# Optimization experiments

Measured on AMD Instinct MI355X. Metric: run time of the kernel, lower is better.

## Reference

```python
import jax, jax.numpy as jnp
import numpy as np

HIDDEN = 1024
B, S = 4, 2048

def setup_inputs() -> dict:
    key = jax.random.key(0)
    k1, k2 = jax.random.split(key)
    hidden_states = jax.random.normal(k1, (B, S, HIDDEN), dtype=jnp.float32)
    # torch nn.Linear weight layout: [out_features, in_features]
    W_proj = jax.random.normal(k2, (3 * HIDDEN, HIDDEN), dtype=jnp.float32) * (1.0 / np.sqrt(HIDDEN))
    b_proj = jnp.zeros((3 * HIDDEN,), dtype=jnp.float32)
    return {"hidden_states": hidden_states, "W_proj": W_proj, "b_proj": b_proj}

def reference(hidden_states, W_proj, b_proj):
    h = hidden_states.shape[-1]
    # fused QKV projection: y = x @ W^T + b
    qkv = jnp.einsum('bsh,oh->bso', hidden_states, W_proj) + b_proj
    q, k, v = jnp.split(qkv, 3, axis=-1)  # each [B,S,H]
    scale = 1.0 / jnp.sqrt(jnp.asarray(h, dtype=q.dtype))
    scores = jnp.einsum('bqh,bkh->bqk', q, k) * scale  # [B,S,S]
    attn = jax.nn.softmax(scores, axis=-1)
    out = jnp.einsum('bqk,bkh->bqh', attn, v)
    return out
```

## Files before the change

kernel.cpp:

```cpp
#include <hip/hip_runtime.h>
#include <stdint.h>

#define HIDDEN 1024
#define BATCH  4
#define SEQ    2048
#define TOKENS (BATCH * SEQ)
#define QKVD   (3 * HIDDEN)

typedef unsigned short u16;
typedef __attribute__((ext_vector_type(8))) short   short8;
typedef __attribute__((ext_vector_type(4))) float   floatx4;

__device__ __forceinline__ u16 f32_bf16_rne(float f) {
    unsigned int u = __float_as_uint(f);
    u += 0x7FFFu + ((u >> 16) & 1u);
    return (u16)(u >> 16);
}

__global__ __launch_bounds__(256) void cvt_bf16_kernel(
        const float* __restrict__ src, u16* __restrict__ dst, int n4) {
    int i = blockIdx.x * 256 + threadIdx.x;
    if (i >= n4) return;
    float4 v = ((const float4*)src)[i];
    ushort4 o;
    o.x = f32_bf16_rne(v.x); o.y = f32_bf16_rne(v.y);
    o.z = f32_bf16_rne(v.z); o.w = f32_bf16_rne(v.w);
    ((ushort4*)dst)[i] = o;
}

template <int EPI>
__global__ __launch_bounds__(256) void gemm_bt(
        const u16* __restrict__ A, const u16* __restrict__ B,
        void* __restrict__ Cv, const float* __restrict__ bias,
        int K, int lda, int ldb, int ldc,
        size_t sA, size_t sB, size_t sC, float scale) {
    __shared__ u16 As[128 * 32];
    __shared__ u16 Bs[128 * 32];

    const int t    = threadIdx.x;
    const int lane = t & 63;
    const int wid  = t >> 6;
    const int bm   = blockIdx.y * 128;
    const int bn   = blockIdx.x * 128;

    const u16* Ab = A + (size_t)blockIdx.z * sA;
    const u16* Bb = B + (size_t)blockIdx.z * sB;

    const int srow = lane >> 2;
    const int scol = ((lane & 3) ^ ((lane >> 3) & 3)) * 8;

    const int wm = (wid >> 1) * 64;
    const int wn = (wid & 1) * 64;
    const int fr = lane & 15;
    const int fc = lane >> 4;
    const int foff = fr * 32 + ((fc ^ ((fr >> 1) & 3)) * 8);

    floatx4 acc[4][4];
#pragma unroll
    for (int i = 0; i < 4; i++)
#pragma unroll
        for (int j = 0; j < 4; j++) acc[i][j] = (floatx4){0.f, 0.f, 0.f, 0.f};

    for (int k0 = 0; k0 < K; k0 += 32) {
        __syncthreads();
#pragma unroll
        for (int j = 0; j < 2; j++) {
            const int chunk = wid * 2 + j;
            const int rt = chunk * 16 + srow;
            const u16* ga = Ab + (size_t)(bm + rt) * lda + (k0 + scol);
            __builtin_amdgcn_global_load_lds(
                (const __attribute__((address_space(1))) void*)ga,
                (__attribute__((address_space(3))) void*)(&As[chunk * 512]),
                16, 0, 0);
            const u16* gb = Bb + (size_t)(bn + rt) * ldb + (k0 + scol);
            __builtin_amdgcn_global_load_lds(
                (const __attribute__((address_space(1))) void*)gb,
                (__attribute__((address_space(3))) void*)(&Bs[chunk * 512]),
                16, 0, 0);
        }
        __syncthreads();

        short8 af[4], bf[4];
#pragma unroll
        for (int mi = 0; mi < 4; mi++)
            af[mi] = *(const short8*)&As[((wm >> 4) + mi) * 512 + foff];
#pragma unroll
        for (int ni = 0; ni < 4; ni++)
            bf[ni] = *(const short8*)&Bs[((wn >> 4) + ni) * 512 + foff];
#pragma unroll
        for (int mi = 0; mi < 4; mi++)
#pragma unroll
            for (int ni = 0; ni < 4; ni++)
                acc[mi][ni] = __builtin_amdgcn_mfma_f32_16x16x32_bf16(
                    af[mi], bf[ni], acc[mi][ni], 0, 0, 0);
    }

    const int crow0 = bm + wm + (lane >> 4) * 4;
    const int ccol0 = bn + wn + fr;
    const size_t coff = (size_t)blockIdx.z * sC;

    if (EPI == 0) {
        u16* C = (u16*)Cv;
        float bv[4];
#pragma unroll
        for (int ni = 0; ni < 4; ni++) bv[ni] = bias[ccol0 + ni * 16];
#pragma unroll
        for (int mi = 0; mi < 4; mi++)
#pragma unroll
            for (int ni = 0; ni < 4; ni++)
#pragma unroll
                for (int r = 0; r < 4; r++)
                    C[coff + (size_t)(crow0 + mi * 16 + r) * ldc + (ccol0 + ni * 16)] =
                        f32_bf16_rne(acc[mi][ni][r] + bv[ni]);
    } else {
        float* C = (float*)Cv;
#pragma unroll
        for (int mi = 0; mi < 4; mi++)
#pragma unroll
            for (int ni = 0; ni < 4; ni++)
#pragma unroll
                for (int r = 0; r < 4; r++) {
                    float v = acc[mi][ni][r];
                    if (EPI == 1) v *= scale;
                    C[coff + (size_t)(crow0 + mi * 16 + r) * ldc + (ccol0 + ni * 16)] = v;
                }
    }
}

__global__ __launch_bounds__(256) void softmax_kernel(
        const float* __restrict__ S, u16* __restrict__ P) {
    __shared__ float redm[4];
    __shared__ float reds[4];
    const size_t base = (size_t)blockIdx.x * SEQ;
    const int t = threadIdx.x, lane = t & 63, wid = t >> 6;
    const float4* src = (const float4*)(S + base);
    float4 a = src[t], b = src[t + 256];

    float m = fmaxf(fmaxf(fmaxf(a.x, a.y), fmaxf(a.z, a.w)),
                    fmaxf(fmaxf(b.x, b.y), fmaxf(b.z, b.w)));
#pragma unroll
    for (int off = 32; off; off >>= 1) m = fmaxf(m, __shfl_xor(m, off, 64));
    if (lane == 0) redm[wid] = m;
    __syncthreads();
    m = fmaxf(fmaxf(redm[0], redm[1]), fmaxf(redm[2], redm[3]));

    float e[8];
    e[0] = __expf(a.x - m); e[1] = __expf(a.y - m);
    e[2] = __expf(a.z - m); e[3] = __expf(a.w - m);
    e[4] = __expf(b.x - m); e[5] = __expf(b.y - m);
    e[6] = __expf(b.z - m); e[7] = __expf(b.w - m);
    float s = e[0] + e[1] + e[2] + e[3] + e[4] + e[5] + e[6] + e[7];
#pragma unroll
    for (int off = 32; off; off >>= 1) s += __shfl_xor(s, off, 64);
    if (lane == 0) reds[wid] = s;
    __syncthreads();
    s = reds[0] + reds[1] + reds[2] + reds[3];
    const float r = 1.f / s;

    ushort4* dst = (ushort4*)(P + base);
    ushort4 o0, o1;
    o0.x = f32_bf16_rne(e[0] * r); o0.y = f32_bf16_rne(e[1] * r);
    o0.z = f32_bf16_rne(e[2] * r); o0.w = f32_bf16_rne(e[3] * r);
    o1.x = f32_bf16_rne(e[4] * r); o1.y = f32_bf16_rne(e[5] * r);
    o1.z = f32_bf16_rne(e[6] * r); o1.w = f32_bf16_rne(e[7] * r);
    dst[t] = o0;
    dst[t + 256] = o1;
}

__global__ __launch_bounds__(256) void transposeV_kernel(
        const u16* __restrict__ qkv, u16* __restrict__ Vt) {
    __shared__ u16 tile[64][66];
    const int b = blockIdx.z;
    const int s0 = blockIdx.x * 64, h0 = blockIdx.y * 64;
    const int t = threadIdx.x;
    const int c = t & 63, r4 = t >> 6;
#pragma unroll
    for (int i = 0; i < 16; i++) {
        int sl = i * 4 + r4;
        tile[sl][c] = qkv[(size_t)(b * SEQ + s0 + sl) * QKVD + 2 * HIDDEN + h0 + c];
    }
    __syncthreads();
#pragma unroll
    for (int i = 0; i < 16; i++) {
        int hl = i * 4 + r4;
        Vt[(size_t)(b * HIDDEN + h0 + hl) * SEQ + s0 + c] = tile[c][hl];
    }
}

extern "C" void kernel_launch(void* const* d_in, const int* in_sizes, int n_in,
                              void* d_out, int out_size, void* d_ws, size_t ws_size,
                              hipStream_t stream) {
    const float* x    = (const float*)d_in[0];
    const float* W    = (const float*)d_in[1];
    const float* bias = (const float*)d_in[2];
    float* out = (float*)d_out;

    u16* Xb  = (u16*)d_ws;
    u16* Wb  = Xb + (size_t)TOKENS * HIDDEN;
    u16* qkv = Wb + (size_t)QKVD * HIDDEN;
    float* scores = (float*)(qkv + (size_t)TOKENS * QKVD);
    u16* P  = (u16*)(scores + (size_t)BATCH * SEQ * SEQ);
    u16* Vt = P + (size_t)BATCH * SEQ * SEQ;

    cvt_bf16_kernel<<<TOKENS * HIDDEN / 4 / 256, 256, 0, stream>>>(x, Xb, TOKENS * HIDDEN / 4);
    cvt_bf16_kernel<<<QKVD * HIDDEN / 4 / 256, 256, 0, stream>>>(W, Wb, QKVD * HIDDEN / 4);

    gemm_bt<0><<<dim3(QKVD / 128, TOKENS / 128, 1), 256, 0, stream>>>(
        Xb, Wb, qkv, bias, HIDDEN, HIDDEN, HIDDEN, QKVD, 0, 0, 0, 1.f);

    gemm_bt<1><<<dim3(SEQ / 128, SEQ / 128, BATCH), 256, 0, stream>>>(
        qkv, qkv + HIDDEN, scores, nullptr, HIDDEN, QKVD, QKVD, SEQ,
        (size_t)SEQ * QKVD, (size_t)SEQ * QKVD, (size_t)SEQ * SEQ, 0.03125f);

    softmax_kernel<<<BATCH * SEQ, 256, 0, stream>>>(scores, P);

    transposeV_kernel<<<dim3(SEQ / 64, HIDDEN / 64, BATCH), 256, 0, stream>>>(qkv, Vt);

    gemm_bt<2><<<dim3(HIDDEN / 128, SEQ / 128, BATCH), 256, 0, stream>>>(
        P, Vt, out, nullptr, SEQ, SEQ, SEQ, HIDDEN,
        (size_t)SEQ * SEQ, (size_t)HIDDEN * SEQ, (size_t)SEQ * HIDDEN, 1.f);
}
```

Baseline: 308.2 us.

## Double-buffer LDS tiles in GEMM to overlap global loads with MFMA

Doubles the A/B shared-memory tiles in the shared GEMM kernel. The next K-slice is now prefetched with direct global-to-LDS loads while MFMAs run on the current slice, which drops one barrier per iteration. Per-thread global base pointers are hoisted out of the loop. This is meant to hide global load latency in all three GEMMs. The cost is twice the LDS per block, which may lower occupancy.

```diff
diff --git a/kernel.cpp b/kernel.cpp
--- a/kernel.cpp
+++ b/kernel.cpp
@@ -34,8 +34,8 @@
         void* __restrict__ Cv, const float* __restrict__ bias,
         int K, int lda, int ldb, int ldc,
         size_t sA, size_t sB, size_t sC, float scale) {
-    __shared__ u16 As[128 * 32];
-    __shared__ u16 Bs[128 * 32];
+    __shared__ u16 As[2][128 * 32];
+    __shared__ u16 Bs[2][128 * 32];
 
     const int t    = threadIdx.x;
     const int lane = t & 63;
@@ -55,44 +55,54 @@
     const int fc = lane >> 4;
     const int foff = fr * 32 + ((fc ^ ((fr >> 1) & 3)) * 8);
 
+    const int c0 = wid * 2, c1 = wid * 2 + 1;
+    const u16* gA0 = Ab + (size_t)(bm + c0 * 16 + srow) * lda + scol;
+    const u16* gA1 = Ab + (size_t)(bm + c1 * 16 + srow) * lda + scol;
+    const u16* gB0 = Bb + (size_t)(bn + c0 * 16 + srow) * ldb + scol;
+    const u16* gB1 = Bb + (size_t)(bn + c1 * 16 + srow) * ldb + scol;
+
+    auto stage = [&](int buf, int k0) {
+        __builtin_amdgcn_global_load_lds(
+            (const __attribute__((address_space(1))) void*)(gA0 + k0),
+            (__attribute__((address_space(3))) void*)(&As[buf][c0 * 512]), 16, 0, 0);
+        __builtin_amdgcn_global_load_lds(
+            (const __attribute__((address_space(1))) void*)(gB0 + k0),
+            (__attribute__((address_space(3))) void*)(&Bs[buf][c0 * 512]), 16, 0, 0);
+        __builtin_amdgcn_global_load_lds(
+            (const __attribute__((address_space(1))) void*)(gA1 + k0),
+            (__attribute__((address_space(3))) void*)(&As[buf][c1 * 512]), 16, 0, 0);
+        __builtin_amdgcn_global_load_lds(
+            (const __attribute__((address_space(1))) void*)(gB1 + k0),
+            (__attribute__((address_space(3))) void*)(&Bs[buf][c1 * 512]), 16, 0, 0);
+    };
+
     floatx4 acc[4][4];
 #pragma unroll
     for (int i = 0; i < 4; i++)
 #pragma unroll
         for (int j = 0; j < 4; j++) acc[i][j] = (floatx4){0.f, 0.f, 0.f, 0.f};
 
+    stage(0, 0);
+
+    int cur = 0;
     for (int k0 = 0; k0 < K; k0 += 32) {
         __syncthreads();
-#pragma unroll
-        for (int j = 0; j < 2; j++) {
-            const int chunk = wid * 2 + j;
-            const int rt = chunk * 16 + srow;
-            const u16* ga = Ab + (size_t)(bm + rt) * lda + (k0 + scol);
-            __builtin_amdgcn_global_load_lds(
-                (const __attribute__((address_space(1))) void*)ga,
-                (__attribute__((address_space(3))) void*)(&As[chunk * 512]),
-                16, 0, 0);
-            const u16* gb = Bb + (size_t)(bn + rt) * ldb + (k0 + scol);
-            __builtin_amdgcn_global_load_lds(
-                (const __attribute__((address_space(1))) void*)gb,
-                (__attribute__((address_space(3))) void*)(&Bs[chunk * 512]),
-                16, 0, 0);
-        }
-        __syncthreads();
+        if (k0 + 32 < K) stage(cur ^ 1, k0 + 32);
 
         short8 af[4], bf[4];
 #pragma unroll
         for (int mi = 0; mi < 4; mi++)
-            af[mi] = *(const short8*)&As[((wm >> 4) + mi) * 512 + foff];
+            af[mi] = *(const short8*)&As[cur][((wm >> 4) + mi) * 512 + foff];
 #pragma unroll
         for (int ni = 0; ni < 4; ni++)
-            bf[ni] = *(const short8*)&Bs[((wn >> 4) + ni) * 512 + foff];
+            bf[ni] = *(const short8*)&Bs[cur][((wn >> 4) + ni) * 512 + foff];
 #pragma unroll
         for (int mi = 0; mi < 4; mi++)
 #pragma unroll
             for (int ni = 0; ni < 4; ni++)
                 acc[mi][ni] = __builtin_amdgcn_mfma_f32_16x16x32_bf16(
                     af[mi], bf[ni], acc[mi][ni], 0, 0, 0);
+        cur ^= 1;
     }
 
     const int crow0 = bm + wm + (lane >> 4) * 4;
```

New measurement: 291.8 us. 1.06x faster.
